# Optimization experiments

Hardware: AMD Instinct MI355X
Metric: run time of the kernel (lower is better)

## Reference

```python
import jax, jax.numpy as jnp
import numpy as np

B, IN_FEATURES, UNITS, BITS = 64, 1024, 1024, 8


def setup_inputs() -> dict:
    key = jax.random.key(0)
    k1, k2, k3 = jax.random.split(key, 3)
    # Quantized integer activations stored as float32 (TF code does int math).
    x = jax.random.randint(k1, (B, IN_FEATURES), 0, 16).astype(jnp.float32)
    # Low-bit integer weights: BITS-bit signed magnitude, |w| < 4**(BITS//2).
    kernel = jax.random.randint(k2, (IN_FEATURES, UNITS), -128, 128).astype(jnp.float32)
    bias = jax.random.randint(k3, (UNITS,), -32, 32).astype(jnp.float32)
    return {"x": x, "kernel": kernel, "bias": bias, "bits": BITS}


def reference(x, kernel, bias, bits):
    # Faithful vectorized version of the TF bit-serial quantized matmul.
    # TF per-feature loop is vectorized over the input-feature axis; the
    # small fixed loop over 2-bit weight chunks is kept (bits//2 iterations).
    nchunks = bits // 2
    sgn = jnp.sign(kernel)            # (In, U)
    wa = jnp.abs(kernel)              # (In, U)
    x3 = x[:, :, None]                # (B, In, 1)
    d = jnp.zeros((x.shape[0], x.shape[1], kernel.shape[1]), x.dtype)  # (B, In, U)
    for _ in range(nchunks):
        c = (wa % 4.0) * sgn          # current 2-bit chunk, re-signed
        d = d + x3 * c[None, :, :]
        wa = jnp.trunc(wa / 4.0)      # tf.cast(w/4, int32): trunc toward 0 (w >= 0)
        d = jnp.trunc(d / 4.0)        # tf.cast(dim1/4, int32): trunc toward 0
    res = d.sum(axis=1)               # (B, U), accumulation over input features
    return jax.nn.relu(res + bias)    # activation == 'relu' branch
```

## Files before the change

### kernel.cpp

```cpp
#include <hip/hip_runtime.h>

#define IN_F   1024
#define UNITS  1024
#define BDIM   64
#define NCH    8
#define CHUNK  128
#define BG     4


__global__ __launch_bounds__(256) void partial_kernel(
    const float* __restrict__ x, const float* __restrict__ K,
    float* __restrict__ ws)
{
    const int bid = blockIdx.x;
    const int jt = bid & 3;
    const int bg = (bid >> 2) & 15;
    const int ic = bid >> 6;
    const int tid = threadIdx.x;
    const int j  = jt * 256 + tid;
    const int b0 = bg * BG;
    const int i0 = ic * CHUNK;

    __shared__ float xs[CHUNK * BG];
    for (int t = tid; t < CHUNK * BG; t += 256) {
        const int bb = t >> 7;
        const int ii = t & 127;
        xs[ii * BG + bb] = x[(b0 + bb) * IN_F + i0 + ii] * (1.0f / 256.0f);
    }
    __syncthreads();

    float acc0 = 0.f, acc1 = 0.f, acc2 = 0.f, acc3 = 0.f;
    const float* kp = K + (size_t)i0 * UNITS + j;
#pragma unroll 8
    for (int i = 0; i < CHUNK; ++i) {
        const float k = kp[(size_t)i * UNITS];
        const float4 xv = *(const float4*)&xs[i * BG];
        acc0 += truncf(xv.x * k);
        acc1 += truncf(xv.y * k);
        acc2 += truncf(xv.z * k);
        acc3 += truncf(xv.w * k);
    }

    float* wp = ws + ((size_t)ic * BDIM + b0) * UNITS + j;
    wp[0 * UNITS] = acc0;
    wp[1 * UNITS] = acc1;
    wp[2 * UNITS] = acc2;
    wp[3 * UNITS] = acc3;
}

__global__ __launch_bounds__(256) void reduce_kernel(
    const float* __restrict__ ws, const float* __restrict__ bias,
    float* __restrict__ out)
{
    const int idx = blockIdx.x * 256 + threadIdx.x;
    const int j4 = idx & 255;
    const int b  = idx >> 8;

    const float4* p = (const float4*)ws + (size_t)b * (UNITS / 4) + j4;
    float4 s = make_float4(0.f, 0.f, 0.f, 0.f);
#pragma unroll
    for (int c = 0; c < NCH; ++c) {
        const float4 v = p[(size_t)c * BDIM * (UNITS / 4)];
        s.x += v.x; s.y += v.y; s.z += v.z; s.w += v.w;
    }
    const float4 bv = ((const float4*)bias)[j4];
    s.x = fmaxf(s.x + bv.x, 0.f);
    s.y = fmaxf(s.y + bv.y, 0.f);
    s.z = fmaxf(s.z + bv.z, 0.f);
    s.w = fmaxf(s.w + bv.w, 0.f);
    ((float4*)out)[idx] = s;
}

extern "C" void kernel_launch(void* const* d_in, const int* in_sizes, int n_in,
                              void* d_out, int out_size, void* d_ws, size_t ws_size,
                              hipStream_t stream) {
    const float* x    = (const float*)d_in[0];
    const float* K    = (const float*)d_in[1];
    const float* bias = (const float*)d_in[2];
    float* out = (float*)d_out;
    float* ws  = (float*)d_ws;

    partial_kernel<<<512, 256, 0, stream>>>(x, K, ws);
    reduce_kernel<<<64, 256, 0, stream>>>(ws, bias, out);
}
```

Before: 73.25 us.

## Fuse split-K partial sums and reduction into one kernel via LDS

Replaces the two-kernel split-K scheme (partials written to global workspace, then a separate reduce kernel) with a single kernel. Each block now covers 64 output units by 4 batch rows, and its 8 waves each take one eighth of the input-feature range. The waves' partial sums are combined in shared memory before bias and relu are applied. This removes one launch and the workspace round trip. In exchange each block stages all 1024 features of x in LDS, the grid drops to 256 blocks, and each K load is now only 64 floats wide per wave row.

```diff
diff --git a/kernel.cpp b/kernel.cpp
--- a/kernel.cpp
+++ b/kernel.cpp
@@ -3,72 +3,66 @@
 #define IN_F   1024
 #define UNITS  1024
 #define BDIM   64
-#define NCH    8
-#define CHUNK  128
-#define BG     4
+#define TJ     64
+#define TB     4
+#define NW     8
+#define WI     (IN_F / NW)
 
 
-__global__ __launch_bounds__(256) void partial_kernel(
+__global__ __launch_bounds__(512) void fused_kernel(
     const float* __restrict__ x, const float* __restrict__ K,
-    float* __restrict__ ws)
+    const float* __restrict__ bias, float* __restrict__ out)
 {
-    const int bid = blockIdx.x;
-    const int jt = bid & 3;
-    const int bg = (bid >> 2) & 15;
-    const int ic = bid >> 6;
-    const int tid = threadIdx.x;
-    const int j  = jt * 256 + tid;
-    const int b0 = bg * BG;
-    const int i0 = ic * CHUNK;
+    const int bid  = blockIdx.x;
+    const int jt   = bid & 15;
+    const int bg   = bid >> 4;
+    const int tid  = threadIdx.x;
+    const int w    = tid >> 6;
+    const int lane = tid & 63;
+    const int j0   = jt * TJ;
+    const int b0   = bg * TB;
 
-    __shared__ float xs[CHUNK * BG];
-    for (int t = tid; t < CHUNK * BG; t += 256) {
-        const int bb = t >> 7;
-        const int ii = t & 127;
-        xs[ii * BG + bb] = x[(b0 + bb) * IN_F + i0 + ii] * (1.0f / 256.0f);
+    __shared__ float xs[IN_F * TB];
+
+    for (int idx = tid; idx < IN_F * TB; idx += 512) {
+        const int bb = idx & 3;
+        const int ii = idx >> 2;
+        xs[idx] = x[(b0 + bb) * IN_F + ii] * (1.0f / 256.0f);
     }
     __syncthreads();
 
     float acc0 = 0.f, acc1 = 0.f, acc2 = 0.f, acc3 = 0.f;
-    const float* kp = K + (size_t)i0 * UNITS + j;
+    const int i0 = w * WI;
+    const float*  kp = K + (size_t)i0 * UNITS + j0 + lane;
+    const float4* xp = (const float4*)&xs[i0 * TB];
 #pragma unroll 8
-    for (int i = 0; i < CHUNK; ++i) {
-        const float k = kp[(size_t)i * UNITS];
-        const float4 xv = *(const float4*)&xs[i * BG];
+    for (int i = 0; i < WI; ++i) {
+        const float  k  = kp[(size_t)i * UNITS];
+        const float4 xv = xp[i];
         acc0 += truncf(xv.x * k);
         acc1 += truncf(xv.y * k);
         acc2 += truncf(xv.z * k);
         acc3 += truncf(xv.w * k);
     }
 
-    float* wp = ws + ((size_t)ic * BDIM + b0) * UNITS + j;
-    wp[0 * UNITS] = acc0;
-    wp[1 * UNITS] = acc1;
-    wp[2 * UNITS] = acc2;
-    wp[3 * UNITS] = acc3;
-}
+    __syncthreads();
+    float* psum = xs;
+    psum[w * 256 + 0 * 64 + lane] = acc0;
+    psum[w * 256 + 1 * 64 + lane] = acc1;
+    psum[w * 256 + 2 * 64 + lane] = acc2;
+    psum[w * 256 + 3 * 64 + lane] = acc3;
+    __syncthreads();
 
-__global__ __launch_bounds__(256) void reduce_kernel(
-    const float* __restrict__ ws, const float* __restrict__ bias,
-    float* __restrict__ out)
-{
-    const int idx = blockIdx.x * 256 + threadIdx.x;
-    const int j4 = idx & 255;
-    const int b  = idx >> 8;
-
-    const float4* p = (const float4*)ws + (size_t)b * (UNITS / 4) + j4;
-    float4 s = make_float4(0.f, 0.f, 0.f, 0.f);
+    if (tid < 256) {
+        const int b = tid >> 6;
+        const int j = tid & 63;
+        float s = 0.f;
 #pragma unroll
-    for (int c = 0; c < NCH; ++c) {
-        const float4 v = p[(size_t)c * BDIM * (UNITS / 4)];
-        s.x += v.x; s.y += v.y; s.z += v.z; s.w += v.w;
+        for (int ww = 0; ww < NW; ++ww)
+            s += psum[ww * 256 + b * 64 + j];
+        s += bias[j0 + j];
+        out[(b0 + b) * UNITS + j0 + j] = fmaxf(s, 0.f);
     }
-    const float4 bv = ((const float4*)bias)[j4];
-    s.x = fmaxf(s.x + bv.x, 0.f);
-    s.y = fmaxf(s.y + bv.y, 0.f);
-    s.z = fmaxf(s.z + bv.z, 0.f);
-    s.w = fmaxf(s.w + bv.w, 0.f);
-    ((float4*)out)[idx] = s;
 }
 
 extern "C" void kernel_launch(void* const* d_in, const int* in_sizes, int n_in,
@@ -78,8 +72,6 @@
     const float* K    = (const float*)d_in[1];
     const float* bias = (const float*)d_in[2];
     float* out = (float*)d_out;
-    float* ws  = (float*)d_ws;
 
-    partial_kernel<<<512, 256, 0, stream>>>(x, K, ws);
-    reduce_kernel<<<64, 256, 0, stream>>>(ws, bias, out);
+    fused_kernel<<<256, 512, 0, stream>>>(x, K, bias, out);
 }
```

Result: faster. 69.75 us (-4.8%).
